# Kernel tuning notes

Measured on AMD Instinct MI355X. Metric: run time of the kernel, lower is better.

Reference implementation:

```python
import jax, jax.numpy as jnp
import numpy as np

LEVELS = 16
FEATURES = 2
HASHMAP_SIZE = 524288
BASE_RES = 16
PER_LEVEL_SCALE = 1.3819

_P1, _P2, _P3 = np.uint32(73856093), np.uint32(19349663), np.uint32(83492791)
# 8 trilinear corner offsets, bit order (x, y, z)
_OFFSETS = np.array([[ox, oy, oz] for ox in (0, 1) for oy in (0, 1) for oz in (0, 1)], dtype=np.int32)


def setup_inputs() -> dict:
    key = jax.random.key(0)
    kx, kt = jax.random.split(key)
    x = jax.random.uniform(kx, (2000000, 3), dtype=jnp.float32)
    tables = jax.random.normal(kt, (LEVELS, HASHMAP_SIZE, FEATURES), dtype=jnp.float32) * 0.01
    return {"x": x, "tables": tables}


def _hash_coords(corners_u32):
    # corners_u32: [N, 8, 3] uint32; spatial hash with uint32 wraparound.
    h = (corners_u32[..., 0] * _P1) ^ (corners_u32[..., 1] * _P2) ^ (corners_u32[..., 2] * _P3)
    return (h % np.uint32(HASHMAP_SIZE)).astype(jnp.int32)  # [N, 8]


def _encode(x, tables):
    offsets_i = jnp.asarray(_OFFSETS)                 # [8, 3] int32
    offsets_f = offsets_i.astype(x.dtype)             # [8, 3]
    embeds = []
    for l in range(LEVELS):
        res = int(BASE_RES * PER_LEVEL_SCALE ** l)
        pos = x * res                                  # [N, 3]
        pos_floor = jnp.floor(pos)
        w = pos - pos_floor                            # [N, 3] trilinear weights
        base = pos_floor.astype(jnp.int32)             # non-negative (x in [0,1])
        corners = (base[:, None, :] + offsets_i).astype(jnp.uint32)  # [N, 8, 3]
        idx = _hash_coords(corners)                    # [N, 8]
        vals = tables[l][idx]                          # [N, 8, F] gather
        # weight per corner = prod over axes of (w if offset else 1-w)
        wgt = jnp.prod(offsets_f * w[:, None, :] + (1.0 - offsets_f) * (1.0 - w[:, None, :]), axis=-1)  # [N, 8]
        embeds.append(jnp.einsum('nc,ncf->nf', wgt, vals))  # [N, F]
    return jnp.concatenate(embeds, axis=-1)           # [N, LEVELS*F]


def reference(x, tables):
    return _encode(x, tables)
```

## Files before the change

kernel.cpp:

```cpp
#include <hip/hip_runtime.h>
#include <stdint.h>

#define LEVELS 16
#define FEAT 2
#define TABLE_SIZE 524288
#define TMASK (TABLE_SIZE - 1)

typedef float f32x2 __attribute__((ext_vector_type(2)));
typedef float f32x4 __attribute__((ext_vector_type(4)));
typedef float f32x4u __attribute__((ext_vector_type(4), aligned(8)));

__device__ __constant__ int kRes[LEVELS] = {
    16, 22, 30, 42, 58, 80, 111, 153, 212, 294, 406, 561, 775, 1072, 1481, 2047
};

#define P1 73856093u
#define P2 19349663u
#define P3 83492791u

#define D0 17
#define N0 4913
#define D1 23
#define N1 12167
#define D2 31
#define N2 29791
#define D3 43
#define N3 79507
#define D4 59
#define N4 205379
#define D5 81
#define N5 531441
#define NDENSE5 (N0 + N1 + N2 + N3 + N4)
#define NDENSE6 (NDENSE5 + N5)

__device__ __constant__ int   kDD[6]   = { D0, D1, D2, D3, D4, D5 };
__device__ __constant__ int   kDOff[6] = { 0, N0, N0+N1, N0+N1+N2, N0+N1+N2+N3, NDENSE5 };
__device__ __constant__ float kDRes[6] = { 16.0f, 22.0f, 30.0f, 42.0f, 58.0f, 80.0f };
__device__ __constant__ int   kDCum[7] = { 0, N0, N0+N1, N0+N1+N2, N0+N1+N2+N3, NDENSE5, NDENSE6 };

__global__ __launch_bounds__(256) void remap_kernel(
    const float* __restrict__ tables,
    f32x2* __restrict__ dense,
    int total)
{
    const int d = blockIdx.x * 256 + threadIdx.x;
    if (d >= total) return;
    int l = 0;
#pragma unroll
    for (int k = 1; k < 6; ++k)
        if (d >= kDCum[k]) l = k;
    const int D   = kDD[l];
    const int rel = d - kDCum[l];
    const uint32_t bx = rel / (D * D);
    const uint32_t r  = rel - bx * (D * D);
    const uint32_t by = r / D;
    const uint32_t bz = r - by * D;
    const uint32_t slot = ((bx * P1) ^ (by * P2) ^ (bz * P3)) & TMASK;
    const f32x2* __restrict__ tab = reinterpret_cast<const f32x2*>(tables) + (size_t)l * TABLE_SIZE;
    dense[d] = tab[slot];
}

__global__ __launch_bounds__(256) void encode_dense_kernel(
    const float* __restrict__ x,
    const f32x2* __restrict__ dense,
    f32x2* __restrict__ ws,
    int n, int ndlev)
{
    const int blk = blockIdx.x;
    const int t   = threadIdx.x;
    const int p0  = blk * 512;

    __shared__ float sx[512 * 3];
    const long long total3 = (long long)n * 3;
    const long long gbase  = (long long)p0 * 3;
#pragma unroll
    for (int k = 0; k < 6; ++k) {
        long long g = gbase + k * 256 + t;
        sx[k * 256 + t] = (g < total3) ? __builtin_nontemporal_load(x + g) : 0.0f;
    }
    __syncthreads();

    const float px[2] = { sx[3 * t + 0],          sx[3 * (t + 256) + 0] };
    const float py[2] = { sx[3 * t + 1],          sx[3 * (t + 256) + 1] };
    const float pz[2] = { sx[3 * t + 2],          sx[3 * (t + 256) + 2] };

    for (int l = 0; l < ndlev; ++l) {
        const int   D    = kDD[l];
        const int   DD   = D * D;
        const float resf = kDRes[l];
        const f32x2* __restrict__ tabd = dense + kDOff[l];

        int   base[2];
        float wxa[2], wya[2], wza[2];
#pragma unroll
        for (int s = 0; s < 2; ++s) {
            const float fx = px[s] * resf;
            const float fy = py[s] * resf;
            const float fz = pz[s] * resf;
            const float flx = floorf(fx), fly = floorf(fy), flz = floorf(fz);
            wxa[s] = fx - flx; wya[s] = fy - fly; wza[s] = fz - flz;
            base[s] = ((int)flx * D + (int)fly) * D + (int)flz;
        }

        f32x4u v[2][4];
#pragma unroll
        for (int s = 0; s < 2; ++s)
#pragma unroll
            for (int p = 0; p < 4; ++p) {
                const int off = ((p & 2) ? DD : 0) + ((p & 1) ? D : 0);
                v[s][p] = *reinterpret_cast<const f32x4u*>(tabd + base[s] + off);
            }

#pragma unroll
        for (int s = 0; s < 2; ++s) {
            const float wx = wxa[s], wy = wya[s], wz = wza[s];
            const float ux = 1.0f - wx, uy = 1.0f - wy, uz = 1.0f - wz;
            float f0 = 0.0f, f1 = 0.0f;
#pragma unroll
            for (int p = 0; p < 4; ++p) {
                const float wxy = ((p & 2) ? wx : ux) * ((p & 1) ? wy : uy);
                f0 = fmaf(wxy, fmaf(uz, v[s][p].x, wz * v[s][p].z), f0);
                f1 = fmaf(wxy, fmaf(uz, v[s][p].y, wz * v[s][p].w), f1);
            }
            const int i = p0 + s * 256 + t;
            if (i < n) {
                f32x2 r; r.x = f0; r.y = f1;
                __builtin_nontemporal_store(r, ws + (size_t)l * n + i);
            }
        }
    }
}

__global__ __launch_bounds__(256) void encode_level_kernel(
    const float* __restrict__ x,
    const float* __restrict__ tables,
    f32x2* __restrict__ ws,
    int n, int nb, int l0)
{
    const int l   = l0 + blockIdx.x / nb;
    const int blk = blockIdx.x - (l - l0) * nb;
    const int t   = threadIdx.x;
    const int p0  = blk * 512;

    __shared__ float sx[512 * 3];
    const long long total3 = (long long)n * 3;
    const long long gbase  = (long long)p0 * 3;
#pragma unroll
    for (int k = 0; k < 6; ++k) {
        long long g = gbase + k * 256 + t;
        sx[k * 256 + t] = (g < total3) ? __builtin_nontemporal_load(x + g) : 0.0f;
    }
    __syncthreads();

    const float resf = (float)kRes[l];
    const f32x2* __restrict__ tab = reinterpret_cast<const f32x2*>(tables) + (size_t)l * TABLE_SIZE;

    uint32_t idx[2][8];
    float    wgt[2][8];
#pragma unroll
    for (int s = 0; s < 2; ++s) {
        const int tp = s * 256 + t;
        const float fx = sx[3 * tp + 0] * resf;
        const float fy = sx[3 * tp + 1] * resf;
        const float fz = sx[3 * tp + 2] * resf;
        const float flx = floorf(fx), fly = floorf(fy), flz = floorf(fz);
        const float wx = fx - flx, wy = fy - fly, wz = fz - flz;
        const float ux = 1.0f - wx, uy = 1.0f - wy, uz = 1.0f - wz;
        const uint32_t hx0 = (uint32_t)(int)flx * P1, hx1 = hx0 + P1;
        const uint32_t hy0 = (uint32_t)(int)fly * P2, hy1 = hy0 + P2;
        const uint32_t hz0 = (uint32_t)(int)flz * P3, hz1 = hz0 + P3;
#pragma unroll
        for (int c = 0; c < 8; ++c) {
            const uint32_t hx = (c & 4) ? hx1 : hx0;
            const uint32_t hy = (c & 2) ? hy1 : hy0;
            const uint32_t hz = (c & 1) ? hz1 : hz0;
            idx[s][c] = (hx ^ hy ^ hz) & TMASK;
            wgt[s][c] = ((c & 4) ? wx : ux) * ((c & 2) ? wy : uy) * ((c & 1) ? wz : uz);
        }
    }

    f32x2 v[2][8];
#pragma unroll
    for (int s = 0; s < 2; ++s)
#pragma unroll
        for (int c = 0; c < 8; ++c)
            v[s][c] = tab[idx[s][c]];

#pragma unroll
    for (int s = 0; s < 2; ++s) {
        float f0 = 0.0f, f1 = 0.0f;
#pragma unroll
        for (int c = 0; c < 8; ++c) {
            f0 = fmaf(wgt[s][c], v[s][c].x, f0);
            f1 = fmaf(wgt[s][c], v[s][c].y, f1);
        }
        const int i = p0 + s * 256 + t;
        if (i < n) {
            f32x2 r; r.x = f0; r.y = f1;
            __builtin_nontemporal_store(r, ws + (size_t)l * n + i);
        }
    }
}

__global__ __launch_bounds__(256) void transpose_kernel(
    const f32x2* __restrict__ ws,
    float* __restrict__ out,
    int n)
{
    __shared__ float s[256 * 33];
    const int t  = threadIdx.x;
    const int p0 = blockIdx.x * 256;
    const int m  = min(256, n - p0);

    if (t < m) {
#pragma unroll
        for (int l = 0; l < LEVELS; ++l) {
            const f32x2 e = __builtin_nontemporal_load(ws + (size_t)l * n + p0 + t);
            s[t * 33 + 2 * l + 0] = e.x;
            s[t * 33 + 2 * l + 1] = e.y;
        }
    }
    __syncthreads();

    const int nchunk = m * 8;
    f32x4* __restrict__ o4 = reinterpret_cast<f32x4*>(out) + (size_t)p0 * 8;
#pragma unroll
    for (int j = 0; j < 8; ++j) {
        const int cl = j * 256 + t;
        if (cl < nchunk) {
            const int p = cl >> 3, ch = cl & 7;
            f32x4 q;
            q.x = s[p * 33 + ch * 4 + 0];
            q.y = s[p * 33 + ch * 4 + 1];
            q.z = s[p * 33 + ch * 4 + 2];
            q.w = s[p * 33 + ch * 4 + 3];
            __builtin_nontemporal_store(q, o4 + cl);
        }
    }
}

__global__ __launch_bounds__(256) void hashgrid_enc_kernel(
    const float* __restrict__ x,
    const float* __restrict__ tables,
    float* __restrict__ out,
    int n)
{
    __shared__ float sx[256 * 3];
    const int t = threadIdx.x;
    const int block0 = blockIdx.x * 256;
    const long long total3 = (long long)n * 3;
    const long long gbase = (long long)block0 * 3;
#pragma unroll
    for (int k = 0; k < 3; ++k) {
        long long g = gbase + k * 256 + t;
        sx[k * 256 + t] = (g < total3) ? x[g] : 0.0f;
    }
    __syncthreads();
    const int i = block0 + t;
    if (i >= n) return;
    const float px = sx[3 * t + 0];
    const float py = sx[3 * t + 1];
    const float pz = sx[3 * t + 2];
    float outv[2 * LEVELS];
#pragma unroll
    for (int l = 0; l < LEVELS; ++l) {
        const float resf = (float)kRes[l];
        const float fx = px * resf, fy = py * resf, fz = pz * resf;
        const float flx = floorf(fx), fly = floorf(fy), flz = floorf(fz);
        const float wx = fx - flx, wy = fy - fly, wz = fz - flz;
        const float ux = 1.0f - wx, uy = 1.0f - wy, uz = 1.0f - wz;
        const uint32_t hx0 = (uint32_t)(int)flx * P1, hx1 = hx0 + P1;
        const uint32_t hy0 = (uint32_t)(int)fly * P2, hy1 = hy0 + P2;
        const uint32_t hz0 = (uint32_t)(int)flz * P3, hz1 = hz0 + P3;
        const float* __restrict__ tab = tables + (size_t)l * (TABLE_SIZE * FEAT);
        float f0 = 0.0f, f1 = 0.0f;
#pragma unroll
        for (int c = 0; c < 8; ++c) {
            const uint32_t hx = (c & 4) ? hx1 : hx0;
            const uint32_t hy = (c & 2) ? hy1 : hy0;
            const uint32_t hz = (c & 1) ? hz1 : hz0;
            const uint32_t idx = (hx ^ hy ^ hz) & TMASK;
            const float2 v = *reinterpret_cast<const float2*>(tab + (size_t)idx * FEAT);
            const float w = ((c & 4) ? wx : ux) * ((c & 2) ? wy : uy) * ((c & 1) ? wz : uz);
            f0 = fmaf(w, v.x, f0);
            f1 = fmaf(w, v.y, f1);
        }
        outv[2 * l + 0] = f0;
        outv[2 * l + 1] = f1;
    }
    float4* __restrict__ o4 = reinterpret_cast<float4*>(out + (size_t)i * (2 * LEVELS));
#pragma unroll
    for (int k = 0; k < 8; ++k) {
        o4[k] = make_float4(outv[4 * k + 0], outv[4 * k + 1],
                            outv[4 * k + 2], outv[4 * k + 3]);
    }
}

extern "C" void kernel_launch(void* const* d_in, const int* in_sizes, int n_in,
                              void* d_out, int out_size, void* d_ws, size_t ws_size,
                              hipStream_t stream) {
    const float* x = (const float*)d_in[0];
    const float* tables = (const float*)d_in[1];
    float* out = (float*)d_out;
    const int n = in_sizes[0] / 3;

    const size_t ws_elems = (size_t)LEVELS * (size_t)n;
    const size_t needA = (ws_elems + NDENSE6 + 2) * sizeof(f32x2);
    const size_t needB = (ws_elems + NDENSE5 + 2) * sizeof(f32x2);

    if (ws_size >= needB) {
        const int  planA  = (ws_size >= needA);
        const int  ndlev  = planA ? 6 : 5;
        const int  l0     = planA ? 6 : 5;
        const int  total  = planA ? NDENSE6 : NDENSE5;
        f32x2* ws    = (f32x2*)d_ws;
        f32x2* dense = ws + ws_elems;

        hipLaunchKernelGGL(remap_kernel, dim3((total + 255) / 256), dim3(256), 0, stream,
                           tables, dense, total);

        const int nb512 = (n + 511) / 512;
        hipLaunchKernelGGL(encode_dense_kernel, dim3(nb512), dim3(256), 0, stream,
                           x, dense, ws, n, ndlev);
        hipLaunchKernelGGL(encode_level_kernel, dim3(nb512 * (LEVELS - l0)), dim3(256), 0, stream,
                           x, tables, ws, n, nb512, l0);

        const int nb256 = (n + 255) / 256;
        hipLaunchKernelGGL(transpose_kernel, dim3(nb256), dim3(256), 0, stream,
                           ws, out, n);
    } else {
        const int nb = (n + 255) / 256;
        hipLaunchKernelGGL(hashgrid_enc_kernel, dim3(nb), dim3(256), 0, stream,
                           x, tables, out, n);
    }
}
```

Before: 1.048 ms.

## Fuse dense-level encoding into the final transpose kernel

Removes the separate dense-level encode kernel and computes the coarse levels directly inside the final transpose/output kernel, writing them straight into shared memory instead of round-tripping through the workspace. This drops one kernel launch and the write-then-reread of the dense-level results (about a third of the workspace traffic). Lookup tables become constexpr and the kernel is templated on the dense-level count so the level loop fully unrolls with immediate constants. In exchange the finalize kernel does more work per thread and uses more registers, which may lower its occupancy.

```diff
diff --git a/kernel.cpp b/kernel.cpp
--- a/kernel.cpp
+++ b/kernel.cpp
@@ -33,10 +33,10 @@
 #define NDENSE5 (N0 + N1 + N2 + N3 + N4)
 #define NDENSE6 (NDENSE5 + N5)
 
-__device__ __constant__ int   kDD[6]   = { D0, D1, D2, D3, D4, D5 };
-__device__ __constant__ int   kDOff[6] = { 0, N0, N0+N1, N0+N1+N2, N0+N1+N2+N3, NDENSE5 };
-__device__ __constant__ float kDRes[6] = { 16.0f, 22.0f, 30.0f, 42.0f, 58.0f, 80.0f };
-__device__ __constant__ int   kDCum[7] = { 0, N0, N0+N1, N0+N1+N2, N0+N1+N2+N3, NDENSE5, NDENSE6 };
+constexpr int   cDD[6]   = { D0, D1, D2, D3, D4, D5 };
+constexpr int   cDOff[6] = { 0, N0, N0+N1, N0+N1+N2, N0+N1+N2+N3, NDENSE5 };
+constexpr float cDRes[6] = { 16.0f, 22.0f, 30.0f, 42.0f, 58.0f, 80.0f };
+constexpr int   cDCum[7] = { 0, N0, N0+N1, N0+N1+N2, N0+N1+N2+N3, NDENSE5, NDENSE6 };
 
 __global__ __launch_bounds__(256) void remap_kernel(
     const float* __restrict__ tables,
@@ -48,9 +48,9 @@
     int l = 0;
 #pragma unroll
     for (int k = 1; k < 6; ++k)
-        if (d >= kDCum[k]) l = k;
-    const int D   = kDD[l];
-    const int rel = d - kDCum[l];
+        if (d >= cDCum[k]) l = k;
+    const int D   = cDD[l];
+    const int rel = d - cDCum[l];
     const uint32_t bx = rel / (D * D);
     const uint32_t r  = rel - bx * (D * D);
     const uint32_t by = r / D;
@@ -58,77 +58,6 @@
     const uint32_t slot = ((bx * P1) ^ (by * P2) ^ (bz * P3)) & TMASK;
     const f32x2* __restrict__ tab = reinterpret_cast<const f32x2*>(tables) + (size_t)l * TABLE_SIZE;
     dense[d] = tab[slot];
-}
-
-__global__ __launch_bounds__(256) void encode_dense_kernel(
-    const float* __restrict__ x,
-    const f32x2* __restrict__ dense,
-    f32x2* __restrict__ ws,
-    int n, int ndlev)
-{
-    const int blk = blockIdx.x;
-    const int t   = threadIdx.x;
-    const int p0  = blk * 512;
-
-    __shared__ float sx[512 * 3];
-    const long long total3 = (long long)n * 3;
-    const long long gbase  = (long long)p0 * 3;
-#pragma unroll
-    for (int k = 0; k < 6; ++k) {
-        long long g = gbase + k * 256 + t;
-        sx[k * 256 + t] = (g < total3) ? __builtin_nontemporal_load(x + g) : 0.0f;
-    }
-    __syncthreads();
-
-    const float px[2] = { sx[3 * t + 0],          sx[3 * (t + 256) + 0] };
-    const float py[2] = { sx[3 * t + 1],          sx[3 * (t + 256) + 1] };
-    const float pz[2] = { sx[3 * t + 2],          sx[3 * (t + 256) + 2] };
-
-    for (int l = 0; l < ndlev; ++l) {
-        const int   D    = kDD[l];
-        const int   DD   = D * D;
-        const float resf = kDRes[l];
-        const f32x2* __restrict__ tabd = dense + kDOff[l];
-
-        int   base[2];
-        float wxa[2], wya[2], wza[2];
-#pragma unroll
-        for (int s = 0; s < 2; ++s) {
-            const float fx = px[s] * resf;
-            const float fy = py[s] * resf;
-            const float fz = pz[s] * resf;
-            const float flx = floorf(fx), fly = floorf(fy), flz = floorf(fz);
-            wxa[s] = fx - flx; wya[s] = fy - fly; wza[s] = fz - flz;
-            base[s] = ((int)flx * D + (int)fly) * D + (int)flz;
-        }
-
-        f32x4u v[2][4];
-#pragma unroll
-        for (int s = 0; s < 2; ++s)
-#pragma unroll
-            for (int p = 0; p < 4; ++p) {
-                const int off = ((p & 2) ? DD : 0) + ((p & 1) ? D : 0);
-                v[s][p] = *reinterpret_cast<const f32x4u*>(tabd + base[s] + off);
-            }
-
-#pragma unroll
-        for (int s = 0; s < 2; ++s) {
-            const float wx = wxa[s], wy = wya[s], wz = wza[s];
-            const float ux = 1.0f - wx, uy = 1.0f - wy, uz = 1.0f - wz;
-            float f0 = 0.0f, f1 = 0.0f;
-#pragma unroll
-            for (int p = 0; p < 4; ++p) {
-                const float wxy = ((p & 2) ? wx : ux) * ((p & 1) ? wy : uy);
-                f0 = fmaf(wxy, fmaf(uz, v[s][p].x, wz * v[s][p].z), f0);
-                f1 = fmaf(wxy, fmaf(uz, v[s][p].y, wz * v[s][p].w), f1);
-            }
-            const int i = p0 + s * 256 + t;
-            if (i < n) {
-                f32x2 r; r.x = f0; r.y = f1;
-                __builtin_nontemporal_store(r, ws + (size_t)l * n + i);
-            }
-        }
-    }
 }
 
 __global__ __launch_bounds__(256) void encode_level_kernel(
@@ -202,22 +131,74 @@
     }
 }
 
-__global__ __launch_bounds__(256) void transpose_kernel(
+template<int NDLEV>
+__global__ __launch_bounds__(256) void finalize_kernel(
+    const float* __restrict__ x,
+    const f32x2* __restrict__ dense,
     const f32x2* __restrict__ ws,
     float* __restrict__ out,
     int n)
 {
     __shared__ float s[256 * 33];
+    __shared__ float sx[256 * 3];
     const int t  = threadIdx.x;
     const int p0 = blockIdx.x * 256;
     const int m  = min(256, n - p0);
 
+    const long long total3 = (long long)n * 3;
+    const long long gbase  = (long long)p0 * 3;
+#pragma unroll
+    for (int k = 0; k < 3; ++k) {
+        long long g = gbase + k * 256 + t;
+        sx[k * 256 + t] = (g < total3) ? __builtin_nontemporal_load(x + g) : 0.0f;
+    }
+    __syncthreads();
+
     if (t < m) {
-#pragma unroll
-        for (int l = 0; l < LEVELS; ++l) {
-            const f32x2 e = __builtin_nontemporal_load(ws + (size_t)l * n + p0 + t);
-            s[t * 33 + 2 * l + 0] = e.x;
-            s[t * 33 + 2 * l + 1] = e.y;
+        const int i = p0 + t;
+        constexpr int NH = LEVELS - NDLEV;
+
+        f32x2 h[NH];
+#pragma unroll
+        for (int j = 0; j < NH; ++j)
+            h[j] = __builtin_nontemporal_load(ws + (size_t)(NDLEV + j) * n + i);
+
+        const float px = sx[3 * t + 0];
+        const float py = sx[3 * t + 1];
+        const float pz = sx[3 * t + 2];
+
+#pragma unroll
+        for (int l = 0; l < NDLEV; ++l) {
+            const int   D    = cDD[l];
+            const int   DD   = D * D;
+            const float resf = cDRes[l];
+            const f32x2* __restrict__ tabd = dense + cDOff[l];
+            const float fx = px * resf, fy = py * resf, fz = pz * resf;
+            const float flx = floorf(fx), fly = floorf(fy), flz = floorf(fz);
+            const float wx = fx - flx, wy = fy - fly, wz = fz - flz;
+            const float ux = 1.0f - wx, uy = 1.0f - wy, uz = 1.0f - wz;
+            const int base = ((int)flx * D + (int)fly) * D + (int)flz;
+
+            f32x4u v[4];
+#pragma unroll
+            for (int p = 0; p < 4; ++p) {
+                const int off = ((p & 2) ? DD : 0) + ((p & 1) ? D : 0);
+                v[p] = *reinterpret_cast<const f32x4u*>(tabd + base + off);
+            }
+            float f0 = 0.0f, f1 = 0.0f;
+#pragma unroll
+            for (int p = 0; p < 4; ++p) {
+                const float wxy = ((p & 2) ? wx : ux) * ((p & 1) ? wy : uy);
+                f0 = fmaf(wxy, fmaf(uz, v[p].x, wz * v[p].z), f0);
+                f1 = fmaf(wxy, fmaf(uz, v[p].y, wz * v[p].w), f1);
+            }
+            s[t * 33 + 2 * l + 0] = f0;
+            s[t * 33 + 2 * l + 1] = f1;
+        }
+#pragma unroll
+        for (int j = 0; j < NH; ++j) {
+            s[t * 33 + 2 * (NDLEV + j) + 0] = h[j].x;
+            s[t * 33 + 2 * (NDLEV + j) + 1] = h[j].y;
         }
     }
     __syncthreads();
@@ -309,10 +290,9 @@
     const size_t needB = (ws_elems + NDENSE5 + 2) * sizeof(f32x2);
 
     if (ws_size >= needB) {
-        const int  planA  = (ws_size >= needA);
-        const int  ndlev  = planA ? 6 : 5;
-        const int  l0     = planA ? 6 : 5;
-        const int  total  = planA ? NDENSE6 : NDENSE5;
+        const int planA = (ws_size >= needA);
+        const int l0    = planA ? 6 : 5;
+        const int total = planA ? NDENSE6 : NDENSE5;
         f32x2* ws    = (f32x2*)d_ws;
         f32x2* dense = ws + ws_elems;
 
@@ -320,14 +300,17 @@
                            tables, dense, total);
 
         const int nb512 = (n + 511) / 512;
-        hipLaunchKernelGGL(encode_dense_kernel, dim3(nb512), dim3(256), 0, stream,
-                           x, dense, ws, n, ndlev);
         hipLaunchKernelGGL(encode_level_kernel, dim3(nb512 * (LEVELS - l0)), dim3(256), 0, stream,
                            x, tables, ws, n, nb512, l0);
 
         const int nb256 = (n + 255) / 256;
-        hipLaunchKernelGGL(transpose_kernel, dim3(nb256), dim3(256), 0, stream,
-                           ws, out, n);
+        if (planA) {
+            hipLaunchKernelGGL((finalize_kernel<6>), dim3(nb256), dim3(256), 0, stream,
+                               x, dense, ws, out, n);
+        } else {
+            hipLaunchKernelGGL((finalize_kernel<5>), dim3(nb256), dim3(256), 0, stream,
+                               x, dense, ws, out, n);
+        }
     } else {
         const int nb = (n + 255) / 256;
         hipLaunchKernelGGL(hashgrid_enc_kernel, dim3(nb), dim3(256), 0, stream,
```

Measured after the change: 1.020 ms. -2.6%, faster.
